# Performance work log

Hardware: AMD Instinct MI355X
Metric: run time of the kernel (lower is better)

The kernel has to match this reference:

```python
import jax, jax.numpy as jnp
import numpy as np

B, D, H, W, N = 64, 512, 32, 32, 20
E = 512  # emb_size
TEMP = 10.0


def setup_inputs() -> dict:
    key = jax.random.key(0)
    ks = jax.random.split(key, 16)
    inp = {
        "fvisu": jax.random.normal(ks[0], (B, D, H, W), jnp.float32),
        "fword": jax.random.normal(ks[1], (B, N, D), jnp.float32),
        "context_score": jax.random.uniform(ks[2], (B, N), jnp.float32),
        "fcoord": jax.random.normal(ks[3], (B, 8, H, W), jnp.float32),
        "gest": jax.random.normal(ks[4], (B, 8), jnp.float32),
        "word_mask": jax.random.randint(ks[5], (B, N), 0, 2, jnp.int32),
        # parameters (kaiming-uniform-ish scale)
        "attn_map_w": jax.random.normal(ks[6], (E // 2, D), jnp.float32) * (1.0 / np.sqrt(D)),
        "attn_map_b": jnp.zeros((E // 2,), jnp.float32),
        "attn_score_w": jax.random.normal(ks[7], (1, E // 2), jnp.float32) * (1.0 / np.sqrt(E // 2)),
        "attn_score_b": jnp.zeros((1,), jnp.float32),
        "gamma_w": jax.random.normal(ks[8], (2 * E, D), jnp.float32) * (1.0 / np.sqrt(D)),
        "gamma_b": jnp.zeros((2 * E,), jnp.float32),
        "conv1_w": jax.random.normal(ks[9], (E, D + 8), jnp.float32) * (1.0 / np.sqrt(D + 8)),
        "conv1_b": jnp.zeros((E,), jnp.float32),
    }
    return inp


def mask_softmax(attn_score, word_mask, temp=TEMP):
    # score: (B, N)
    score = jax.nn.softmax(attn_score * temp, axis=1)
    m = word_mask.astype(jnp.int32)
    m = m.at[:, 0].set(0)                      # zero CLS position
    idx = jnp.sum(m, axis=1)                   # index of SEP (post-CLS-zeroing), matches torch loop
    m = m.at[jnp.arange(m.shape[0]), idx].set(0)
    ms = score * m.astype(score.dtype)
    return ms / (jnp.sum(ms, axis=1, keepdims=True) + 1e-8)


def reference(fvisu, fword, context_score, fcoord, gest, word_mask,
              attn_map_w, attn_map_b, attn_score_w, attn_score_b,
              gamma_w, gamma_b, conv1_w, conv1_b):
    # fword: (B, N, D) -> module permutes to (B, D, N)
    fw = jnp.transpose(fword, (0, 2, 1))                      # (B, D, N)
    tile_visu = jnp.mean(fvisu.reshape(B, D, -1), axis=2, keepdims=True)  # (B, D, 1)
    context_tile = tile_visu * fw * context_score[:, None, :]  # (B, D, N)

    # 1x1 Conv1d -> GEMM
    attn_feat = jnp.tanh(jnp.einsum('od,bdn->bon', attn_map_w, context_tile)
                         + attn_map_b[None, :, None])          # (B, E/2, N)
    attn_score = (jnp.einsum('oc,bcn->bon', attn_score_w, attn_feat)[:, 0, :]
                  + attn_score_b[0])                           # (B, N)

    mask_score = mask_softmax(attn_score, word_mask)            # (B, N)
    attn_lang = jnp.einsum('bn,bnd->bd', mask_score, fword)     # (B, D)

    # FiLM parameter decode
    film = attn_lang @ gamma_w.T + gamma_b                      # (B, 2E)
    gammas = jnp.tanh(film[:, :E])[:, :, None, None]
    betas = jnp.tanh(film[:, E:])[:, :, None, None]

    # 1x1 Conv2d on concat(fvisu, fcoord) + InstanceNorm2d (no affine, eps=1e-5)
    x = jnp.concatenate([fvisu, fcoord], axis=1)                # (B, D+8, H, W)
    conv = jnp.einsum('oc,bchw->bohw', conv1_w, x) + conv1_b[None, :, None, None]
    mu = jnp.mean(conv, axis=(2, 3), keepdims=True)
    var = jnp.var(conv, axis=(2, 3), keepdims=True)
    norm = (conv - mu) * jax.lax.rsqrt(var + 1e-5)

    fmodu = jax.nn.relu(gammas * norm + betas)
    fmodu = fvisu + fmodu
    return fmodu, attn_lang, attn_score
```

## Files before the change

kernel.cpp:

```cpp
#include <hip/hip_runtime.h>
#include <math.h>

#define BB 64
#define DD 512
#define HW 1024
#define NN 20
#define EE 512
#define CIN 520
#define KCN 17
#define TEMP_F 10.0f

#define OUT_ALANG (BB*DD*HW)
#define OUT_ASCORE (OUT_ALANG + BB*DD)

typedef __bf16 bf16x8 __attribute__((ext_vector_type(8)));
typedef float f32x4 __attribute__((ext_vector_type(4)));

__device__ __forceinline__ unsigned int pack2bf(float a, float b) {
    unsigned int ua = __builtin_bit_cast(unsigned int, a);
    unsigned int ub = __builtin_bit_cast(unsigned int, b);
    ua += 0x7fffu + ((ua >> 16) & 1u);
    ub += 0x7fffu + ((ub >> 16) & 1u);
    return (ua >> 16) | (ub & 0xffff0000u);
}

__device__ __forceinline__ unsigned short bfr(float x) {
    unsigned int u = __builtin_bit_cast(unsigned int, x);
    u += 0x7fffu + ((u >> 16) & 1u);
    return (unsigned short)(u >> 16);
}

__device__ __forceinline__ float bf2f(unsigned short u) {
    unsigned int x = ((unsigned int)u) << 16;
    return __builtin_bit_cast(float, x);
}

__global__ __launch_bounds__(256) void k_tilevisu(const float* __restrict__ fvisu,
                                                  float* __restrict__ tv) {
    int row = blockIdx.x;
    const float4* p = (const float4*)(fvisu + (size_t)row * HW);
    int tid = threadIdx.x;
    float4 v = p[tid];
    float s = v.x + v.y + v.z + v.w;
    #pragma unroll
    for (int off = 32; off; off >>= 1) s += __shfl_down(s, off, 64);
    __shared__ float part[4];
    if ((tid & 63) == 0) part[tid >> 6] = s;
    __syncthreads();
    if (tid == 0) tv[row] = (part[0] + part[1] + part[2] + part[3]) * (1.0f / HW);
}

__global__ __launch_bounds__(512, 2) void k_convert_x(
    const float* __restrict__ fvisu, const float* __restrict__ fcoord,
    unsigned short* __restrict__ Xf, float* __restrict__ tv) {
    __shared__ unsigned short frag[64][528];
    __shared__ float red[8][8];
    int L = blockIdx.x;
    int kc = L % KCN;
    int b  = L / KCN;
    int t = threadIdx.x;
    int co = t >> 7;
    int tl = t & 127;
    int cbase = kc * 32 + co * 8;
    float sums[8];
    #pragma unroll
    for (int j = 0; j < 8; ++j) sums[j] = 0.f;

    #pragma unroll
    for (int i = 0; i < 2; ++i) {
        int p0 = (tl + 128 * i) * 4;
        float4 f4[8];
        #pragma unroll
        for (int j = 0; j < 8; ++j) {
            int c = cbase + j;
            if (c < DD) {
                f4[j] = *(const float4*)&fvisu[((size_t)b * DD + c) * HW + p0];
            } else if (c < CIN) {
                f4[j] = *(const float4*)&fcoord[((size_t)b * 8 + (c - DD)) * HW + p0];
            } else {
                f4[j] = make_float4(0.f, 0.f, 0.f, 0.f);
            }
        }
        #pragma unroll
        for (int j = 0; j < 8; ++j)
            if (cbase + j < DD) sums[j] += f4[j].x + f4[j].y + f4[j].z + f4[j].w;

        int P = p0 >> 4;
        #pragma unroll
        for (int i2 = 0; i2 < 4; ++i2) {
            uint4 v;
            v.x = pack2bf(((const float*)&f4[0])[i2], ((const float*)&f4[1])[i2]);
            v.y = pack2bf(((const float*)&f4[2])[i2], ((const float*)&f4[3])[i2]);
            v.z = pack2bf(((const float*)&f4[4])[i2], ((const float*)&f4[5])[i2]);
            v.w = pack2bf(((const float*)&f4[6])[i2], ((const float*)&f4[7])[i2]);
            int unit = co * 16 + (p0 & 15) + i2;
            *(uint4*)&frag[P][unit * 8] = v;
        }
    }

    #pragma unroll
    for (int j = 0; j < 8; ++j) {
        float s = sums[j];
        #pragma unroll
        for (int off = 32; off; off >>= 1) s += __shfl_down(s, off, 64);
        sums[j] = s;
    }
    int w = t >> 6, l = t & 63;
    if (l == 0) {
        #pragma unroll
        for (int j = 0; j < 8; ++j) red[w][j] = sums[j];
    }
    __syncthreads();

    #pragma unroll
    for (int fi = 0; fi < 8; ++fi) {
        int f = w * 8 + fi;
        uint4 v = *(const uint4*)&frag[f][l * 8];
        *(uint4*)&Xf[(((size_t)b * 64 + f) * KCN + kc) * 512 + (size_t)l * 8] = v;
    }

    if (t < 32) {
        int j = t & 7, c2 = t >> 3;
        int c = kc * 32 + c2 * 8 + j;
        if (c < DD) tv[(size_t)b * DD + c] = (red[c2 * 2][j] + red[c2 * 2 + 1][j]) * (1.0f / HW);
    }
}

__global__ __launch_bounds__(256) void k_convert_params(
    const float* __restrict__ cw, unsigned short* __restrict__ Wf,
    const float* __restrict__ amw, unsigned short* __restrict__ Whi,
    unsigned short* __restrict__ Wlo,
    const float* __restrict__ gw, float* __restrict__ gwT) {
    int B0 = blockIdx.x;
    int t = threadIdx.x;
    if (B0 < 136) {
        int frag = B0 * 4 + (t >> 6);
        int l = t & 63;
        int M = frag / KCN, kc = frag % KCN;
        int o = M * 16 + (l & 15);
        int k0 = kc * 32 + (l >> 4) * 8;
        float f[8];
        #pragma unroll
        for (int j = 0; j < 8; ++j) {
            int k = k0 + j;
            f[j] = (k < CIN) ? cw[(size_t)o * CIN + k] : 0.f;
        }
        uint4 v;
        v.x = pack2bf(f[0], f[1]);
        v.y = pack2bf(f[2], f[3]);
        v.z = pack2bf(f[4], f[5]);
        v.w = pack2bf(f[6], f[7]);
        *(uint4*)&Wf[(size_t)frag * 512 + (size_t)l * 8] = v;
    } else if (B0 < 200) {
        int fid = (B0 - 136) * 4 + (t >> 6);
        int l = t & 63;
        int o = (fid >> 4) * 16 + (l & 15);
        int k0 = (fid & 15) * 32 + ((l >> 4) & 3) * 8;
        float hi[8], lo[8];
        #pragma unroll
        for (int j = 0; j < 8; ++j) {
            float x = amw[(size_t)o * DD + k0 + j];
            unsigned short h = bfr(x);
            hi[j] = bf2f(h);
            lo[j] = x - hi[j];
        }
        uint4 vh, vl;
        vh.x = pack2bf(hi[0], hi[1]); vh.y = pack2bf(hi[2], hi[3]);
        vh.z = pack2bf(hi[4], hi[5]); vh.w = pack2bf(hi[6], hi[7]);
        vl.x = pack2bf(lo[0], lo[1]); vl.y = pack2bf(lo[2], lo[3]);
        vl.z = pack2bf(lo[4], lo[5]); vl.w = pack2bf(lo[6], lo[7]);
        *(uint4*)&Whi[(size_t)fid * 512 + (size_t)l * 8] = vh;
        *(uint4*)&Wlo[(size_t)fid * 512 + (size_t)l * 8] = vl;
    } else {
        __shared__ float tile[64][65];
        int bt = B0 - 200;
        int rt = bt & 15, kt = bt >> 4;
        int rl = t >> 4;
        int kl = (t & 15) * 4;
        #pragma unroll
        for (int i = 0; i < 4; ++i) {
            int rr = rl + i * 16;
            float4 v = *(const float4*)&gw[(size_t)(rt * 64 + rr) * DD + kt * 64 + kl];
            tile[rr][kl + 0] = v.x; tile[rr][kl + 1] = v.y;
            tile[rr][kl + 2] = v.z; tile[rr][kl + 3] = v.w;
        }
        __syncthreads();
        #pragma unroll
        for (int i = 0; i < 4; ++i) {
            int kk = rl + i * 16;
            float4 v;
            v.x = tile[kl + 0][kk]; v.y = tile[kl + 1][kk];
            v.z = tile[kl + 2][kk]; v.w = tile[kl + 3][kk];
            *(float4*)&gwT[(size_t)(kt * 64 + kk) * 1024 + rt * 64 + kl] = v;
        }
    }
}

__global__ __launch_bounds__(256) void k_attnscore(
    const float* __restrict__ fword, const float* __restrict__ cs,
    const float* __restrict__ tv, const unsigned short* __restrict__ Whi,
    const unsigned short* __restrict__ Wlo, const float* __restrict__ amb,
    const float* __restrict__ asw, const float* __restrict__ asb,
    const int* __restrict__ wmask, float* __restrict__ out_ascore,
    float* __restrict__ out_alang) {
    int b = blockIdx.x;
    __shared__ unsigned short uhi[2][16][64][8];
    __shared__ unsigned short ulo[2][16][64][8];
    __shared__ float scoreP[4][32];
    __shared__ float asc_sh[NN];
    __shared__ float msh[NN];
    int t = threadIdx.x;

    {
        int n = t & 31, kq = t >> 5;
        float csv = (n < NN) ? cs[b * NN + n] : 0.f;
        const float* fwp = fword + ((size_t)b * NN + (n < NN ? n : 0)) * DD;
        const float* tvp = tv + (size_t)b * DD;
        int mt = n >> 4;
        #pragma unroll
        for (int oc = 0; oc < 8; ++oc) {
            int k = kq * 64 + oc * 8;
            float x[8];
            if (n < NN) {
                float4 f0 = *(const float4*)&fwp[k];
                float4 f1 = *(const float4*)&fwp[k + 4];
                float4 t0 = *(const float4*)&tvp[k];
                float4 t1 = *(const float4*)&tvp[k + 4];
                x[0] = f0.x * t0.x * csv; x[1] = f0.y * t0.y * csv;
                x[2] = f0.z * t0.z * csv; x[3] = f0.w * t0.w * csv;
                x[4] = f1.x * t1.x * csv; x[5] = f1.y * t1.y * csv;
                x[6] = f1.z * t1.z * csv; x[7] = f1.w * t1.w * csv;
            } else {
                #pragma unroll
                for (int j = 0; j < 8; ++j) x[j] = 0.f;
            }
            float h[8], lw[8];
            #pragma unroll
            for (int j = 0; j < 8; ++j) {
                h[j] = bf2f(bfr(x[j]));
                lw[j] = x[j] - h[j];
            }
            int ks = k >> 5;
            int l = (n & 15) + ((k >> 3) & 3) * 16;
            uint4 vh, vl;
            vh.x = pack2bf(h[0], h[1]); vh.y = pack2bf(h[2], h[3]);
            vh.z = pack2bf(h[4], h[5]); vh.w = pack2bf(h[6], h[7]);
            vl.x = pack2bf(lw[0], lw[1]); vl.y = pack2bf(lw[2], lw[3]);
            vl.z = pack2bf(lw[4], lw[5]); vl.w = pack2bf(lw[6], lw[7]);
            *(uint4*)&uhi[mt][ks][l][0] = vh;
            *(uint4*)&ulo[mt][ks][l][0] = vl;
        }
    }
    __syncthreads();

    int w = t >> 6, l = t & 63;
    f32x4 acc[2][4];
    #pragma unroll
    for (int mt = 0; mt < 2; ++mt)
        #pragma unroll
        for (int nt = 0; nt < 4; ++nt) acc[mt][nt] = (f32x4){0.f, 0.f, 0.f, 0.f};

    #pragma unroll 4
    for (int ks = 0; ks < 16; ++ks) {
        bf16x8 ah0 = *(const bf16x8*)&uhi[0][ks][l][0];
        bf16x8 ah1 = *(const bf16x8*)&uhi[1][ks][l][0];
        bf16x8 al0 = *(const bf16x8*)&ulo[0][ks][l][0];
        bf16x8 al1 = *(const bf16x8*)&ulo[1][ks][l][0];
        #pragma unroll
        for (int nt = 0; nt < 4; ++nt) {
            size_t fo = ((size_t)((w * 4 + nt) * 16 + ks)) * 512 + (size_t)l * 8;
            bf16x8 bh = *(const bf16x8*)&Whi[fo];
            bf16x8 bl = *(const bf16x8*)&Wlo[fo];
            acc[0][nt] = __builtin_amdgcn_mfma_f32_16x16x32_bf16(ah0, bh, acc[0][nt], 0, 0, 0);
            acc[0][nt] = __builtin_amdgcn_mfma_f32_16x16x32_bf16(al0, bh, acc[0][nt], 0, 0, 0);
            acc[0][nt] = __builtin_amdgcn_mfma_f32_16x16x32_bf16(ah0, bl, acc[0][nt], 0, 0, 0);
            acc[1][nt] = __builtin_amdgcn_mfma_f32_16x16x32_bf16(ah1, bh, acc[1][nt], 0, 0, 0);
            acc[1][nt] = __builtin_amdgcn_mfma_f32_16x16x32_bf16(al1, bh, acc[1][nt], 0, 0, 0);
            acc[1][nt] = __builtin_amdgcn_mfma_f32_16x16x32_bf16(ah1, bl, acc[1][nt], 0, 0, 0);
        }
    }

    float ambv[4], aswv[4];
    #pragma unroll
    for (int nt = 0; nt < 4; ++nt) {
        int o = (w * 4 + nt) * 16 + (l & 15);
        ambv[nt] = amb[o];
        aswv[nt] = asw[o];
    }
    #pragma unroll
    for (int mt = 0; mt < 2; ++mt) {
        #pragma unroll
        for (int j = 0; j < 4; ++j) {
            float p = 0.f;
            #pragma unroll
            for (int nt = 0; nt < 4; ++nt)
                p += aswv[nt] * tanhf(acc[mt][nt][j] + ambv[nt]);
            #pragma unroll
            for (int off = 1; off < 16; off <<= 1) p += __shfl_xor(p, off, 64);
            if ((l & 15) == 0) scoreP[w][mt * 16 + (l >> 4) * 4 + j] = p;
        }
    }
    __syncthreads();
    if (t < NN) {
        float v = scoreP[0][t] + scoreP[1][t] + scoreP[2][t] + scoreP[3][t] + asb[0];
        out_ascore[b * NN + t] = v;
        asc_sh[t] = v;
    }
    __syncthreads();

    if (t == 0) {
        float s[NN];
        float mx = -1e30f;
        for (int n = 0; n < NN; ++n) { s[n] = asc_sh[n] * TEMP_F; mx = fmaxf(mx, s[n]); }
        float se = 0.f;
        for (int n = 0; n < NN; ++n) { s[n] = expf(s[n] - mx); se += s[n]; }
        int m[NN]; int idx = 0;
        for (int n = 0; n < NN; ++n) m[n] = wmask[b * NN + n];
        m[0] = 0;
        for (int n = 0; n < NN; ++n) idx += m[n];
        m[idx] = 0;
        float tot = 0.f;
        for (int n = 0; n < NN; ++n) { float v = (s[n] / se) * (float)m[n]; msh[n] = v; tot += v; }
        float inv = 1.f / (tot + 1e-8f);
        for (int n = 0; n < NN; ++n) msh[n] *= inv;
    }
    __syncthreads();

    #pragma unroll 2
    for (int d = t; d < DD; d += 256) {
        float a = 0.f;
        #pragma unroll
        for (int n = 0; n < NN; ++n) a += msh[n] * fword[((size_t)b * NN + n) * DD + d];
        out_alang[b * DD + d] = a;
    }
}

__global__ __launch_bounds__(256) void k_attnscore_legacy(
    const float* __restrict__ fword, const float* __restrict__ cs,
    const float* __restrict__ tv, const float* __restrict__ amw,
    const float* __restrict__ amb, const float* __restrict__ asw,
    const float* __restrict__ asb, float* __restrict__ out_ascore) {
    int bn = blockIdx.x;
    int b = bn / NN, n = bn % NN;
    __shared__ float u[DD];
    __shared__ float part[4];
    int tid = threadIdx.x;
    float csv = cs[b * NN + n];
    for (int d = tid; d < DD; d += 256)
        u[d] = tv[b * DD + d] * fword[((size_t)b * NN + n) * DD + d] * csv;
    __syncthreads();
    int o = tid;
    const float4* wrow = (const float4*)(amw + (size_t)o * DD);
    const float4* uv = (const float4*)u;
    float dot = 0.f;
    #pragma unroll 4
    for (int i = 0; i < DD / 4; ++i) {
        float4 w4 = wrow[i]; float4 u4 = uv[i];
        dot += w4.x * u4.x + w4.y * u4.y + w4.z * u4.z + w4.w * u4.w;
    }
    float contrib = asw[o] * tanhf(dot + amb[o]);
    #pragma unroll
    for (int off = 32; off; off >>= 1) contrib += __shfl_down(contrib, off, 64);
    if ((tid & 63) == 0) part[tid >> 6] = contrib;
    __syncthreads();
    if (tid == 0) out_ascore[b * NN + n] = part[0] + part[1] + part[2] + part[3] + asb[0];
}

__global__ __launch_bounds__(256) void k_lang_film(
    const float* __restrict__ fword, const int* __restrict__ wmask,
    const float* __restrict__ ascore, const float* __restrict__ gw,
    const float* __restrict__ gb, float* __restrict__ out_alang,
    float* __restrict__ ws_film) {
    int b = blockIdx.x >> 2;
    int qd = blockIdx.x & 3;
    __shared__ float ms[NN];
    __shared__ float al[DD];
    int tid = threadIdx.x;
    if (tid == 0) {
        float s[NN];
        float mx = -1e30f;
        for (int n = 0; n < NN; ++n) { s[n] = ascore[b * NN + n] * TEMP_F; mx = fmaxf(mx, s[n]); }
        float se = 0.f;
        for (int n = 0; n < NN; ++n) { s[n] = expf(s[n] - mx); se += s[n]; }
        int m[NN]; int idx = 0;
        for (int n = 0; n < NN; ++n) m[n] = wmask[b * NN + n];
        m[0] = 0;
        for (int n = 0; n < NN; ++n) idx += m[n];
        m[idx] = 0;
        float tot = 0.f;
        for (int n = 0; n < NN; ++n) { float v = (s[n] / se) * (float)m[n]; ms[n] = v; tot += v; }
        float inv = 1.f / (tot + 1e-8f);
        for (int n = 0; n < NN; ++n) ms[n] *= inv;
    }
    __syncthreads();
    for (int d = tid; d < DD; d += 256) {
        float a = 0.f;
        #pragma unroll
        for (int n = 0; n < NN; ++n) a += ms[n] * fword[((size_t)b * NN + n) * DD + d];
        al[d] = a;
        if (qd == 0) out_alang[b * DD + d] = a;
    }
    __syncthreads();
    {
        int r = qd * 256 + tid;
        const float4* grow = (const float4*)(gw + (size_t)r * DD);
        const float4* av = (const float4*)al;
        float dot = 0.f;
        #pragma unroll 4
        for (int i = 0; i < DD / 4; ++i) {
            float4 g4 = grow[i]; float4 a4 = av[i];
            dot += g4.x * a4.x + g4.y * a4.y + g4.z * a4.z + g4.w * a4.w;
        }
        ws_film[b * 2 * EE + r] = tanhf(dot + gb[r]);
    }
}

__global__ __launch_bounds__(256) void k_film(
    const float* __restrict__ alang, const float* __restrict__ gwT,
    const float* __restrict__ gb, float* __restrict__ ws_film) {
    int b = blockIdx.x >> 2;
    int q = blockIdx.x & 3;
    __shared__ float al[DD];
    int t = threadIdx.x;
    al[t] = alang[b * DD + t];
    al[t + 256] = alang[b * DD + t + 256];
    __syncthreads();
    int r = q * 256 + t;
    float acc = 0.f;
    #pragma unroll 8
    for (int k = 0; k < DD; ++k)
        acc += al[k] * gwT[(size_t)k * 1024 + r];
    ws_film[b * 1024 + r] = tanhf(acc + gb[r]);
}

__global__ __launch_bounds__(512, 2) void k_gemm_in_film(
    const unsigned short* __restrict__ Xf, const unsigned short* __restrict__ Wf,
    const float* __restrict__ film, float* __restrict__ out) {
    __shared__ float sP[8][64];
    __shared__ float qP[8][64];
    __shared__ float st[64][4];
    int L = blockIdx.x;
    int ot = (L >> 3) & 7;
    int b  = (L >> 6) * 8 + (L & 7);
    int t = threadIdx.x;
    int w = t >> 6, l = t & 63;

    const unsigned short* Xw = Xf + ((size_t)b * 64 + w * 8) * (KCN * 512) + (size_t)l * 8;
    const unsigned short* Wb = Wf + (size_t)(ot * 4) * (KCN * 512) + (size_t)l * 8;
    int ot2 = 2 * ot;

    f32x4 acc[4][8];
    #pragma unroll
    for (int m = 0; m < 4; ++m)
        #pragma unroll
        for (int n = 0; n < 8; ++n) acc[m][n] = (f32x4){0.f, 0.f, 0.f, 0.f};

    auto kcof = [&](int j) -> int {
        if (j < 15) return j + (j >= ot2 ? 2 : 0);
        return (j == 15) ? ot2 : (ot2 + 1);
    };
    auto loadB = [&](int j, bf16x8* bf_) {
        int kc = kcof(j);
        #pragma unroll
        for (int i = 0; i < 8; ++i)
            bf_[i] = *(const bf16x8*)(Xw + ((size_t)i * KCN + kc) * 512);
    };
    auto loadA = [&](int j, bf16x8* af) {
        int kc = kcof(j);
        #pragma unroll
        for (int m = 0; m < 4; ++m)
            af[m] = *(const bf16x8*)(Wb + ((size_t)m * KCN + kc) * 512);
    };
    auto compute = [&](const bf16x8* af, const bf16x8* bf_) {
        __builtin_amdgcn_s_setprio(1);
        #pragma unroll
        for (int m = 0; m < 4; ++m)
            #pragma unroll
            for (int n = 0; n < 8; ++n)
                acc[m][n] = __builtin_amdgcn_mfma_f32_16x16x32_bf16(af[m], bf_[n], acc[m][n], 0, 0, 0);
        __builtin_amdgcn_s_setprio(0);
    };

    bf16x8 bA[8], bB[8], aA[4], aB[4];
    loadB(0, bA);
    loadA(0, aA);

    #pragma unroll
    for (int j = 0; j < KCN; ++j) {
        if (j & 1) {
            if (j + 1 < KCN) { loadB(j + 1, bA); loadA(j + 1, aA); }
            compute(aB, bB);
        } else {
            if (j + 1 < KCN) { loadB(j + 1, bB); loadA(j + 1, aB); }
            compute(aA, bA);
        }
    }

    #pragma unroll
    for (int m = 0; m < 4; ++m) {
        #pragma unroll
        for (int j = 0; j < 4; ++j) {
            float s = 0.f, q = 0.f;
            #pragma unroll
            for (int n = 0; n < 8; ++n) { float v = acc[m][n][j]; s += v; q += v * v; }
            #pragma unroll
            for (int off = 1; off < 16; off <<= 1) {
                s += __shfl_xor(s, off, 64);
                q += __shfl_xor(q, off, 64);
            }
            if ((l & 15) == 0) {
                int ol = m * 16 + (l >> 4) * 4 + j;
                sP[w][ol] = s;
                qP[w][ol] = q;
            }
        }
    }
    __syncthreads();
    if (t < 64) {
        float s = 0.f, q = 0.f;
        #pragma unroll
        for (int ww = 0; ww < 8; ++ww) { s += sP[ww][t]; q += qP[ww][t]; }
        float mu = s * (1.0f / HW);
        float var = q * (1.0f / HW) - mu * mu;
        int oc = ot * 64 + t;
        st[t][0] = mu;
        st[t][1] = rsqrtf(var + 1e-5f);
        st[t][2] = film[b * 1024 + oc];
        st[t][3] = film[b * 1024 + 512 + oc];
    }
    __syncthreads();

    float* ob = out + ((size_t)b * DD + ot * 64) * HW;
    int q4 = l >> 4;
    #pragma unroll
    for (int m = 0; m < 4; ++m) {
        int kc_m = ot2 + (m >> 1);
        int lp = ((m & 1) * 2 + (q4 >> 1)) * 16 + (l & 15);
        int uo = lp * 8 + (q4 & 1) * 4;
        #pragma unroll
        for (int n = 0; n < 8; ++n) {
            ushort4 rb = *(const ushort4*)(Xf + ((size_t)b * 64 + w * 8 + n) * (KCN * 512)
                                           + ((size_t)kc_m) * 512 + uo);
            int px = w * 128 + n * 16 + (l & 15);
            #pragma unroll
            for (int jj = 0; jj < 4; ++jj) {
                int ol = m * 16 + q4 * 4 + jj;
                f32x4 sv = *(const f32x4*)&st[ol][0];
                float nrm = (acc[m][n][jj] - sv[0]) * sv[1];
                float rr = sv[2] * nrm + sv[3];
                rr = rr > 0.f ? rr : 0.f;
                float res = bf2f(((const unsigned short*)&rb)[jj]);
                ob[(size_t)ol * HW + px] = res + rr;
            }
        }
    }
}

__global__ __launch_bounds__(256) void k_conv_in_film(
    const float* __restrict__ fvisu, const float* __restrict__ fcoord,
    const float* __restrict__ cw, const float* __restrict__ film,
    float* __restrict__ out) {
    int L = blockIdx.x;
    int b = L & 63;
    int tgt = L >> 6;
    int o0 = tgt * 16;
    int tid = threadIdx.x;
    __shared__ float xs[8][HW];
    __shared__ float red[16][4][2];
    __shared__ float stats[16][2];
    float acc[16][4];
    #pragma unroll
    for (int o = 0; o < 16; ++o)
        #pragma unroll
        for (int j = 0; j < 4; ++j) acc[o][j] = 0.f;

    const float* xb_v = fvisu + (size_t)b * DD * HW;
    const float* xb_c = fcoord + (size_t)b * 8 * HW;

    for (int c0 = 0; c0 < CIN; c0 += 8) {
        #pragma unroll
        for (int i = 0; i < 8; ++i) {
            int c = c0 + i;
            const float* src = (c < DD) ? (xb_v + (size_t)c * HW) : (xb_c + (size_t)(c - DD) * HW);
            ((float4*)xs[i])[tid] = ((const float4*)src)[tid];
        }
        __syncthreads();
        #pragma unroll
        for (int i = 0; i < 8; ++i) {
            float xv[4];
            #pragma unroll
            for (int j = 0; j < 4; ++j) xv[j] = xs[i][tid + 256 * j];
            #pragma unroll
            for (int o = 0; o < 16; ++o) {
                float wv = cw[(size_t)(o0 + o) * CIN + (c0 + i)];
                #pragma unroll
                for (int j = 0; j < 4; ++j) acc[o][j] = fmaf(wv, xv[j], acc[o][j]);
            }
        }
        __syncthreads();
    }
    int lane = tid & 63, wid = tid >> 6;
    #pragma unroll
    for (int o = 0; o < 16; ++o) {
        float s = 0.f, q = 0.f;
        #pragma unroll
        for (int j = 0; j < 4; ++j) { s += acc[o][j]; q += acc[o][j] * acc[o][j]; }
        #pragma unroll
        for (int off = 32; off; off >>= 1) {
            s += __shfl_down(s, off, 64);
            q += __shfl_down(q, off, 64);
        }
        if (lane == 0) { red[o][wid][0] = s; red[o][wid][1] = q; }
    }
    __syncthreads();
    if (tid < 16) {
        float s = red[tid][0][0] + red[tid][1][0] + red[tid][2][0] + red[tid][3][0];
        float q = red[tid][0][1] + red[tid][1][1] + red[tid][2][1] + red[tid][3][1];
        float mu = s * (1.0f / HW);
        float var = q * (1.0f / HW) - mu * mu;
        stats[tid][0] = mu;
        stats[tid][1] = rsqrtf(var + 1e-5f);
    }
    __syncthreads();
    #pragma unroll
    for (int o = 0; o < 16; ++o) {
        int oc = o0 + o;
        float mu = stats[o][0], rs = stats[o][1];
        float g  = film[b * 1024 + oc];
        float be = film[b * 1024 + 512 + oc];
        const float* fv = xb_v + (size_t)oc * HW;
        float* op = out + ((size_t)b * DD + oc) * HW;
        #pragma unroll
        for (int j = 0; j < 4; ++j) {
            int p = tid + 256 * j;
            float nrm = (acc[o][j] - mu) * rs;
            float rr = g * nrm + be;
            rr = rr > 0.f ? rr : 0.f;
            op[p] = fv[p] + rr;
        }
    }
}

extern "C" void kernel_launch(void* const* d_in, const int* in_sizes, int n_in,
                              void* d_out, int out_size, void* d_ws, size_t ws_size,
                              hipStream_t stream) {
    const float* fvisu  = (const float*)d_in[0];
    const float* fword  = (const float*)d_in[1];
    const float* cscore = (const float*)d_in[2];
    const float* fcoord = (const float*)d_in[3];
    const int*   wmask  = (const int*)d_in[5];
    const float* amw    = (const float*)d_in[6];
    const float* amb    = (const float*)d_in[7];
    const float* asw    = (const float*)d_in[8];
    const float* asb    = (const float*)d_in[9];
    const float* gw     = (const float*)d_in[10];
    const float* gb     = (const float*)d_in[11];
    const float* cw     = (const float*)d_in[12];

    float* out = (float*)d_out;
    float* ws_tv   = (float*)d_ws;
    float* ws_film = ws_tv + BB * DD;
    unsigned short* Xf  = (unsigned short*)((char*)d_ws + 393216);
    unsigned short* Wf  = (unsigned short*)((char*)d_ws + 393216 + 71303168);
    unsigned short* Whi = (unsigned short*)((char*)d_ws + 393216 + 71303168 + 557056);
    unsigned short* Wlo = Whi + 131072;
    float* gwT = (float*)((char*)d_ws + 393216 + 71303168 + 557056 + 524288);
    const size_t need = 393216 + 71303168 + 557056 + 524288 + 2097152;

    float* out_alang  = out + OUT_ALANG;
    float* out_ascore = out + OUT_ASCORE;

    if (ws_size >= need) {
        k_convert_params<<<328, 256, 0, stream>>>(cw, Wf, amw, Whi, Wlo, gw, gwT);
        k_convert_x<<<BB * KCN, 512, 0, stream>>>(fvisu, fcoord, Xf, ws_tv);
        k_attnscore<<<BB, 256, 0, stream>>>(fword, cscore, ws_tv, Whi, Wlo, amb, asw, asb,
                                            wmask, out_ascore, out_alang);
        k_film<<<BB * 4, 256, 0, stream>>>(out_alang, gwT, gb, ws_film);
        k_gemm_in_film<<<512, 512, 0, stream>>>(Xf, Wf, ws_film, out);
    } else {
        k_tilevisu<<<BB * DD, 256, 0, stream>>>(fvisu, ws_tv);
        k_attnscore_legacy<<<BB * NN, 256, 0, stream>>>(fword, cscore, ws_tv, amw, amb, asw, asb, out_ascore);
        k_lang_film<<<BB * 4, 256, 0, stream>>>(fword, wmask, out_ascore, gw, gb, out_alang, ws_film);
        k_conv_in_film<<<BB * 32, 256, 0, stream>>>(fvisu, fcoord, cw, ws_film, out);
    }
}
```

Before: 175.6 us.

## Stage conv weight tile in LDS and triple-buffer activation loads

After: 175.4 us. Within noise of the previous version (-0.1%).

```diff
diff --git a/kernel.cpp b/kernel.cpp
--- a/kernel.cpp
+++ b/kernel.cpp
@@ -436,6 +436,7 @@
 __global__ __launch_bounds__(512, 2) void k_gemm_in_film(
     const unsigned short* __restrict__ Xf, const unsigned short* __restrict__ Wf,
     const float* __restrict__ film, float* __restrict__ out) {
+    __shared__ __align__(16) unsigned short als[68 * 512];
     __shared__ float sP[8][64];
     __shared__ float qP[8][64];
     __shared__ float st[64][4];
@@ -446,7 +447,6 @@
     int w = t >> 6, l = t & 63;
 
     const unsigned short* Xw = Xf + ((size_t)b * 64 + w * 8) * (KCN * 512) + (size_t)l * 8;
-    const unsigned short* Wb = Wf + (size_t)(ot * 4) * (KCN * 512) + (size_t)l * 8;
     int ot2 = 2 * ot;
 
     f32x4 acc[4][8];
@@ -465,35 +465,42 @@
         for (int i = 0; i < 8; ++i)
             bf_[i] = *(const bf16x8*)(Xw + ((size_t)i * KCN + kc) * 512);
     };
-    auto loadA = [&](int j, bf16x8* af) {
+    auto compute = [&](int j, const bf16x8* bf_) {
         int kc = kcof(j);
-        #pragma unroll
-        for (int m = 0; m < 4; ++m)
-            af[m] = *(const bf16x8*)(Wb + ((size_t)m * KCN + kc) * 512);
-    };
-    auto compute = [&](const bf16x8* af, const bf16x8* bf_) {
         __builtin_amdgcn_s_setprio(1);
         #pragma unroll
-        for (int m = 0; m < 4; ++m)
+        for (int m = 0; m < 4; ++m) {
+            bf16x8 a = *(const bf16x8*)&als[(size_t)((m * KCN + kc) * 64 + l) * 8];
             #pragma unroll
             for (int n = 0; n < 8; ++n)
-                acc[m][n] = __builtin_amdgcn_mfma_f32_16x16x32_bf16(af[m], bf_[n], acc[m][n], 0, 0, 0);
+                acc[m][n] = __builtin_amdgcn_mfma_f32_16x16x32_bf16(a, bf_[n], acc[m][n], 0, 0, 0);
+        }
         __builtin_amdgcn_s_setprio(0);
     };
 
-    bf16x8 bA[8], bB[8], aA[4], aB[4];
-    loadB(0, bA);
-    loadA(0, aA);
+    bf16x8 b0[8], b1[8], b2[8];
+    loadB(0, b0);
+    loadB(1, b1);
+
+    {
+        const unsigned short* Wbase = Wf + (size_t)(ot * 68) * 512;
+        #pragma unroll
+        for (int i = 0; i < 9; ++i) {
+            int idx = t + i * 512;
+            if (idx < 68 * 64)
+                *(uint4*)&als[(size_t)idx * 8] = *(const uint4*)&Wbase[(size_t)idx * 8];
+        }
+    }
+    __syncthreads();
 
     #pragma unroll
     for (int j = 0; j < KCN; ++j) {
-        if (j & 1) {
-            if (j + 1 < KCN) { loadB(j + 1, bA); loadA(j + 1, aA); }
-            compute(aB, bB);
-        } else {
-            if (j + 1 < KCN) { loadB(j + 1, bB); loadA(j + 1, aB); }
-            compute(aA, bA);
-        }
+        bf16x8* cur = (j % 3 == 0) ? b0 : (j % 3 == 1) ? b1 : b2;
+        if (j + 2 < KCN) {
+            bf16x8* nxt = ((j + 2) % 3 == 0) ? b0 : ((j + 2) % 3 == 1) ? b1 : b2;
+            loadB(j + 2, nxt);
+        }
+        compute(j, cur);
     }
 
     #pragma unroll
```
